# Optimization experiments

Hardware: AMD Instinct MI355X
Metric: run time of the kernel (lower is better)

Reference implementation:

```python
import jax, jax.numpy as jnp
import numpy as np

DEPTH, DIM, M_DIM, K = 3, 16, 16, 8  # depth, emb_dim, EGNN m_dim default, num_nearest_neighbors
LN_EPS = 1e-5


def _gather(x, idx):
    # x: [B,L,...], idx: [B,L,K] -> [B,L,K,...] (per-batch neighbor gather)
    return jax.vmap(lambda xb, ib: xb[ib])(x, idx)


def _lin(k, fi, fo):
    k1, k2 = jax.random.split(k)
    lim = 1.0 / np.sqrt(fi)
    w = jax.random.uniform(k1, (fi, fo), minval=-lim, maxval=lim, dtype=jnp.float32)
    b = jax.random.uniform(k2, (fo,), minval=-lim, maxval=lim, dtype=jnp.float32)
    return w, b


def _stacked(k, fi, fo):
    ws, bs = zip(*[_lin(kk, fi, fo) for kk in jax.random.split(k, DEPTH)])
    return jnp.stack(ws), jnp.stack(bs)


def setup_inputs() -> dict:
    key = jax.random.key(0)
    ks = jax.random.split(key, 16)
    B, L, num_tokens = 16, 1024, 2
    edge_in = 2 * DIM + 1  # feats_i, feats_j, rel_dist
    inp = {}
    inp['coords'] = jax.random.normal(ks[0], (B, L, 3), dtype=jnp.float32) * 3.0
    inp['residues'] = jax.random.randint(ks[1], (B, L), 0, num_tokens)
    inp['lengths'] = jax.random.randint(ks[2], (B,), L // 2, L + 1)
    inp['token_emb'] = jax.random.normal(ks[3], (num_tokens, DIM), dtype=jnp.float32)
    inp['pos_emb'] = jax.random.normal(ks[4], (L, DIM), dtype=jnp.float32)
    inp['edge_w1'], inp['edge_b1'] = _stacked(ks[5], edge_in, edge_in * 2)
    inp['edge_w2'], inp['edge_b2'] = _stacked(ks[6], edge_in * 2, M_DIM)
    inp['coors_w1'], inp['coors_b1'] = _stacked(ks[7], M_DIM, M_DIM * 4)
    inp['coors_w2'], inp['coors_b2'] = _stacked(ks[8], M_DIM * 4, 1)
    inp['ln_g'] = jnp.ones((DEPTH, DIM), jnp.float32)
    inp['ln_b'] = jnp.zeros((DEPTH, DIM), jnp.float32)
    inp['node_w1'], inp['node_b1'] = _stacked(ks[9], DIM + M_DIM, DIM * 2)
    inp['node_w2'], inp['node_b2'] = _stacked(ks[10], DIM * 2, DIM)
    inp['final_w'], inp['final_b'] = _lin(ks[11], DIM, 3)
    return inp


def reference(coords, residues, lengths, token_emb, pos_emb,
              edge_w1, edge_b1, edge_w2, edge_b2,
              coors_w1, coors_b1, coors_w2, coors_b2,
              ln_g, ln_b, node_w1, node_b1, node_w2, node_b2,
              final_w, final_b):
    B, L, _ = coords.shape
    silu = jax.nn.silu
    mask = jnp.arange(L)[None, :] < lengths[:, None]                 # [B,L]
    pair_mask = mask[:, :, None] & mask[:, None, :]                  # [B,L,L]
    eye = jnp.eye(L, dtype=bool)
    # chain adjacency: i <-> i+1 where both endpoints are within length
    r = jnp.arange(L - 1)
    chain = jnp.zeros((L, L), bool).at[r, r + 1].set(True)
    chain = chain | chain.T
    adj = (chain[None] & pair_mask) & ~eye                           # [B,L,L]

    feats = token_emb[residues] + pos_emb[None, :L]                  # [B,L,D]
    coors = coords
    for d in range(DEPTH):
        # pairwise squared distances for kNN ranking (memory-bound)
        rel_dist_full = jnp.sum((coors[:, :, None] - coors[:, None, :]) ** 2, -1)  # [B,L,L]
        ranking = jnp.where(pair_mask, rel_dist_full, 1e5)
        ranking = jnp.where(eye, -1.0, ranking)   # self always selected first
        ranking = jnp.where(adj, 0.0, ranking)    # adjacency edges forced in
        _, idx = jax.lax.top_k(-ranking, K)                           # [B,L,K] smallest
        mask_j = _gather(mask, idx)
        emask = mask[:, :, None] & mask_j                             # [B,L,K] (valid_radius=inf)
        coors_j = _gather(coors, idx)                                 # [B,L,K,3]
        rel_coors = coors[:, :, None] - coors_j                       # [B,L,K,3]
        rel_dist = jnp.sum(rel_coors ** 2, -1, keepdims=True)         # [B,L,K,1]
        feats_j = _gather(feats, idx)                                 # [B,L,K,D]
        feats_i = jnp.broadcast_to(feats[:, :, None], feats_j.shape)
        edge_in = jnp.concatenate([feats_i, feats_j, rel_dist], -1)   # [B,L,K,2D+1]
        h = silu(edge_in @ edge_w1[d] + edge_b1[d])
        m_ij = silu(h @ edge_w2[d] + edge_b2[d])                      # [B,L,K,M]
        # equivariant coordinate update
        w = silu(m_ij @ coors_w1[d] + coors_b1[d]) @ coors_w2[d] + coors_b2[d]
        w = jnp.where(emask[..., None], w, 0.0)[..., 0]               # [B,L,K]
        coors = coors + jnp.einsum('blk,blkc->blc', w, rel_coors)
        # node update (norm_feats=True in EGNN_Network -> LayerNorm)
        m_i = jnp.sum(jnp.where(emask[..., None], m_ij, 0.0), 2)      # [B,L,M]
        mu = feats.mean(-1, keepdims=True)
        var = jnp.mean((feats - mu) ** 2, -1, keepdims=True)
        normed = (feats - mu) / jnp.sqrt(var + LN_EPS) * ln_g[d] + ln_b[d]
        nin = jnp.concatenate([normed, m_i], -1)                      # [B,L,D+M]
        feats = feats + (silu(nin @ node_w1[d] + node_b1[d]) @ node_w2[d] + node_b2[d])
    delta = feats @ final_w + final_b                                 # [B,L,3]
    return delta
```

## Files before the change

### kernel.cpp

```cpp
#include <hip/hip_runtime.h>
#include <math.h>

typedef unsigned long long u64;
typedef unsigned int u32;

#define NB 16
#define SL 1024
#define DIM 16
#define MDIM 16
#define KNN 8
#define EH 66
#define CH 64
#define NHID 32
#define LN_EPS 1e-5f
#define W1T_STRIDE 36

__device__ __forceinline__ float silu_f(float x) {
    return x / (1.0f + __expf(-x));
}

__global__ __launch_bounds__(256) void init_kernel(
    const float* __restrict__ coords, const int* __restrict__ residues,
    const float* __restrict__ token_emb, const float* __restrict__ pos_emb,
    float* __restrict__ coordsA, float* __restrict__ featsA)
{
    const int nid = blockIdx.x * 256 + threadIdx.x;
    if (nid >= NB * SL) return;
    const int l = nid & (SL - 1);
    const int r = residues[nid];
#pragma unroll
    for (int c = 0; c < DIM; ++c)
        featsA[nid * DIM + c] = token_emb[r * DIM + c] + pos_emb[l * DIM + c];
#pragma unroll
    for (int c = 0; c < 3; ++c)
        coordsA[nid * 3 + c] = coords[nid * 3 + c];
}

__global__ __launch_bounds__(256) void pack_kernel(
    const float* __restrict__ ew1, const float* __restrict__ cw1,
    const float* __restrict__ nw1, const float* __restrict__ nw2,
    float* __restrict__ w1t, float* __restrict__ cw1t,
    float* __restrict__ nw1t, float* __restrict__ nw2t)
{
    const int stride = gridDim.x * 256;
    const int t0 = blockIdx.x * 256 + threadIdx.x;
    for (int idx = t0; idx < 3 * EH * 33; idx += stride) {
        int d = idx / (EH * 33); int r = idx - d * EH * 33; int u = r / 33; int c = r - u * 33;
        w1t[(d * EH + u) * W1T_STRIDE + c] = ew1[(d * 33 + c) * EH + u];
    }
    for (int idx = t0; idx < 3 * CH * 16; idx += stride) {
        int d = idx / (CH * 16); int r = idx - d * CH * 16; int t = r >> 4; int v = r & 15;
        cw1t[(d * CH + t) * 16 + v] = cw1[(d * 16 + v) * CH + t];
    }
    for (int idx = t0; idx < 3 * NHID * 32; idx += stride) {
        int d = idx / (NHID * 32); int r = idx - d * NHID * 32; int u = r >> 5; int c = r & 31;
        nw1t[(d * NHID + u) * 32 + c] = nw1[(d * 32 + c) * NHID + u];
    }
    for (int idx = t0; idx < 3 * 16 * 32; idx += stride) {
        int d = idx / (16 * 32); int r = idx - d * 16 * 32; int c = r >> 5; int u = r & 31;
        nw2t[(d * 16 + c) * 32 + u] = nw2[(d * 32 + u) * 16 + c];
    }
}

__device__ __forceinline__ void merge8(u32* a, const u32* bb) {
    u32 c[8];
#pragma unroll
    for (int t = 0; t < 8; ++t) c[t] = min(a[t], bb[7 - t]);
#define MCAS(x, y) { u32 mn = min(c[x], c[y]); u32 mx = max(c[x], c[y]); c[x] = mn; c[y] = mx; }
    MCAS(0, 4) MCAS(1, 5) MCAS(2, 6) MCAS(3, 7)
    MCAS(0, 2) MCAS(1, 3) MCAS(4, 6) MCAS(5, 7)
    MCAS(0, 1) MCAS(2, 3) MCAS(4, 5) MCAS(6, 7)
#undef MCAS
#pragma unroll
    for (int t = 0; t < 8; ++t) a[t] = c[t];
}

__global__ __launch_bounds__(1024) void knn_kernel(
    const float* __restrict__ coords, const int* __restrict__ lengths,
    int* __restrict__ idxbuf)
{
    __shared__ float s_cand[SL * 3];
    __shared__ u32 lists[16][64][9];
    const int tid = threadIdx.x;
    const int b = blockIdx.x >> 4;
    const int i0 = (blockIdx.x & 15) << 6;
    const int len = lengths[b];
    const float* cb = coords + (size_t)b * SL * 3;
    for (int idx = tid; idx < SL * 3; idx += 1024) s_cand[idx] = cb[idx];
    __syncthreads();

    const int wv = tid >> 6;
    const int lane = tid & 63;
    const int i = i0 + lane;
    const bool mi = i < len;
    const float xi = s_cand[i * 3 + 0], yi = s_cand[i * 3 + 1], zi = s_cand[i * 3 + 2];

    u32 lst[8];
#pragma unroll
    for (int t = 0; t < 8; ++t) lst[t] = 0xFFFFFFFFu;

    const int jbase = wv << 6;
#pragma unroll 4
    for (int jj = 0; jj < 64; ++jj) {
        const int j = jbase + jj;
        const float xj = s_cand[j * 3 + 0], yj = s_cand[j * 3 + 1], zj = s_cand[j * 3 + 2];
        const float dx = xi - xj, dy = yi - yj, dz = zi - zj;
        const float dist = dx * dx + dy * dy + dz * dz;
        const bool pm = mi && (j < len);
        float v = pm ? dist : 1e5f;
        v = (pm && (j - i == 1 || i - j == 1)) ? 0.0f : v;
        v = (j == i) ? -1.0f : v;
        u32 bits = __float_as_uint(v);
        bits ^= (u32)((int)bits >> 31) | 0x80000000u;
        const u32 key = (bits & 0xFFFFFC00u) | (u32)j;
#pragma unroll
        for (int p = 7; p >= 1; --p)
            lst[p] = (key < lst[p]) ? ((key < lst[p - 1]) ? lst[p - 1] : key) : lst[p];
        lst[0] = min(key, lst[0]);
    }

#pragma unroll
    for (int t = 0; t < 8; ++t) lists[wv][lane][t] = lst[t];
    __syncthreads();

    if (tid < 512) {
        const int p = tid >> 6, q = tid & 63;
        u32 a[8], bb[8];
#pragma unroll
        for (int t = 0; t < 8; ++t) { a[t] = lists[2 * p][q][t]; bb[t] = lists[2 * p + 1][q][t]; }
        merge8(a, bb);
#pragma unroll
        for (int t = 0; t < 8; ++t) lists[2 * p][q][t] = a[t];
    }
    __syncthreads();
    if (tid < 256) {
        const int p = tid >> 6, q = tid & 63;
        u32 a[8], bb[8];
#pragma unroll
        for (int t = 0; t < 8; ++t) { a[t] = lists[4 * p][q][t]; bb[t] = lists[4 * p + 2][q][t]; }
        merge8(a, bb);
#pragma unroll
        for (int t = 0; t < 8; ++t) lists[4 * p][q][t] = a[t];
    }
    __syncthreads();
    if (tid < 128) {
        const int p = tid >> 6, q = tid & 63;
        u32 a[8], bb[8];
#pragma unroll
        for (int t = 0; t < 8; ++t) { a[t] = lists[8 * p][q][t]; bb[t] = lists[8 * p + 4][q][t]; }
        merge8(a, bb);
#pragma unroll
        for (int t = 0; t < 8; ++t) lists[8 * p][q][t] = a[t];
    }
    __syncthreads();
    if (tid < 64) {
        const int q = tid;
        u32 a[8], bb[8];
#pragma unroll
        for (int t = 0; t < 8; ++t) { a[t] = lists[0][q][t]; bb[t] = lists[8][q][t]; }
        merge8(a, bb);
        const size_t node = (size_t)b * SL + i0 + q;
        int4 r0 = make_int4((int)(a[0] & 1023u), (int)(a[1] & 1023u), (int)(a[2] & 1023u), (int)(a[3] & 1023u));
        int4 r1 = make_int4((int)(a[4] & 1023u), (int)(a[5] & 1023u), (int)(a[6] & 1023u), (int)(a[7] & 1023u));
        ((int4*)idxbuf)[node * 2 + 0] = r0;
        ((int4*)idxbuf)[node * 2 + 1] = r1;
    }
}

__global__ __launch_bounds__(256, 4) void layer_kernel(
    const int d,
    const float* __restrict__ coordsIn, float* __restrict__ coordsOut,
    const float* __restrict__ featsIn, float* __restrict__ featsOut,
    const int* __restrict__ idxbuf, const int* __restrict__ lengths,
    const float* __restrict__ w1t, const float* __restrict__ g_eb1,
    const float* __restrict__ g_ew2, const float* __restrict__ g_eb2,
    const float* __restrict__ cw1t, const float* __restrict__ g_cb1,
    const float* __restrict__ g_cw2, const float* __restrict__ g_cb2,
    const float* __restrict__ g_lng, const float* __restrict__ g_lnb,
    const float* __restrict__ nw1t, const float* __restrict__ g_nb1,
    const float* __restrict__ nw2t, const float* __restrict__ g_nb2)
{
    __shared__ float s_w1[EH * 36];
    __shared__ float s_w2e[EH * 16];
    __shared__ float s_cw1[CH * 16];
    __shared__ float s_cw2v[CH];
    __shared__ float s_nw1[NHID * 36];
    __shared__ float s_nw2[16 * 36];
    __shared__ float s_eb1[EH], s_eb2[16], s_cb1[CH];
    __shared__ float s_lng[16], s_lnb[16], s_nb1[32], s_nb2[16];
    __shared__ float s_cb2v;
    __shared__ __align__(16) float s_ex[2 * 64 * 20];

    const int tid = threadIdx.x;
    for (int t = tid; t < EH * 36; t += 256) s_w1[t] = w1t[d * EH * 36 + t];
    for (int t = tid; t < EH * 16; t += 256) s_w2e[t] = g_ew2[d * EH * 16 + t];
    for (int t = tid; t < CH * 16; t += 256) s_cw1[t] = cw1t[d * CH * 16 + t];
    for (int t = tid; t < NHID * 32; t += 256) s_nw1[(t >> 5) * 36 + (t & 31)] = nw1t[d * NHID * 32 + t];
    for (int t = tid; t < 16 * 32; t += 256) s_nw2[(t >> 5) * 36 + (t & 31)] = nw2t[d * 16 * 32 + t];
    if (tid < CH) { s_cw2v[tid] = g_cw2[d * CH + tid]; s_cb1[tid] = g_cb1[d * CH + tid]; }
    if (tid < EH) s_eb1[tid] = g_eb1[d * EH + tid];
    if (tid < 16) {
        s_eb2[tid] = g_eb2[d * 16 + tid];
        s_lng[tid] = g_lng[d * 16 + tid];
        s_lnb[tid] = g_lnb[d * 16 + tid];
        s_nb2[tid] = g_nb2[d * 16 + tid];
    }
    if (tid < 32) s_nb1[tid] = g_nb1[d * 32 + tid];
    if (tid == 0) s_cb2v = g_cb2[d];

    const int wvid = tid >> 6;
    const int h = wvid & 1;
    const int p = wvid >> 1;
    const int lane = tid & 63;
    const int e = blockIdx.x * 128 + p * 64 + lane;
    const int n = e >> 3;
    const int b = n >> 10;
    const int i = n & (SL - 1);
    const int k = lane & 7;
    const int len = lengths[b];
    const int j = idxbuf[e];
    const bool em = (i < len) && (j < len);

    float fi[16], fj[16];
    {
        const float4* pp = (const float4*)(featsIn + (size_t)n * DIM);
        float4 a = pp[0], c2 = pp[1], c3 = pp[2], c4 = pp[3];
        fi[0]=a.x; fi[1]=a.y; fi[2]=a.z; fi[3]=a.w;
        fi[4]=c2.x; fi[5]=c2.y; fi[6]=c2.z; fi[7]=c2.w;
        fi[8]=c3.x; fi[9]=c3.y; fi[10]=c3.z; fi[11]=c3.w;
        fi[12]=c4.x; fi[13]=c4.y; fi[14]=c4.z; fi[15]=c4.w;
    }
    {
        const float4* pp = (const float4*)(featsIn + ((size_t)b * SL + j) * DIM);
        float4 a = pp[0], c2 = pp[1], c3 = pp[2], c4 = pp[3];
        fj[0]=a.x; fj[1]=a.y; fj[2]=a.z; fj[3]=a.w;
        fj[4]=c2.x; fj[5]=c2.y; fj[6]=c2.z; fj[7]=c2.w;
        fj[8]=c3.x; fj[9]=c3.y; fj[10]=c3.z; fj[11]=c3.w;
        fj[12]=c4.x; fj[13]=c4.y; fj[14]=c4.z; fj[15]=c4.w;
    }
    float ci[3], rel[3];
    {
        const float* cp = coordsIn + (size_t)n * 3;
        const float* cq = coordsIn + ((size_t)b * SL + j) * 3;
        ci[0] = cp[0]; ci[1] = cp[1]; ci[2] = cp[2];
        rel[0] = ci[0] - cq[0]; rel[1] = ci[1] - cq[1]; rel[2] = ci[2] - cq[2];
    }
    const float rd = fmaf(rel[0], rel[0], fmaf(rel[1], rel[1], rel[2] * rel[2]));

    __syncthreads();

    const int ub = h * 33;
    float macc[16];
#pragma unroll
    for (int v = 0; v < 16; ++v) macc[v] = h ? 0.0f : s_eb2[v];
#pragma unroll 3
    for (int uu = 0; uu < 33; ++uu) {
        const float* wr = &s_w1[(ub + uu) * 36];
        float h0 = s_eb1[ub + uu], h1 = 0.f, h2 = 0.f, h3 = 0.f;
#pragma unroll
        for (int c = 0; c < 16; c += 4) {
            h0 = fmaf(fi[c + 0], wr[c + 0], h0);
            h1 = fmaf(fi[c + 1], wr[c + 1], h1);
            h2 = fmaf(fi[c + 2], wr[c + 2], h2);
            h3 = fmaf(fi[c + 3], wr[c + 3], h3);
        }
#pragma unroll
        for (int c = 0; c < 16; c += 4) {
            h0 = fmaf(fj[c + 0], wr[16 + c + 0], h0);
            h1 = fmaf(fj[c + 1], wr[16 + c + 1], h1);
            h2 = fmaf(fj[c + 2], wr[16 + c + 2], h2);
            h3 = fmaf(fj[c + 3], wr[16 + c + 3], h3);
        }
        h0 = fmaf(rd, wr[32], h0);
        const float hh = silu_f((h0 + h1) + (h2 + h3));
        const float* w2r = &s_w2e[(ub + uu) * 16];
#pragma unroll
        for (int v = 0; v < 16; ++v) macc[v] = fmaf(hh, w2r[v], macc[v]);
    }

    float4* exq = (float4*)&s_ex[((p << 6) + lane) * 20];
    if (h) {
        exq[0] = make_float4(macc[0], macc[1], macc[2], macc[3]);
        exq[1] = make_float4(macc[4], macc[5], macc[6], macc[7]);
        exq[2] = make_float4(macc[8], macc[9], macc[10], macc[11]);
        exq[3] = make_float4(macc[12], macc[13], macc[14], macc[15]);
    }
    __syncthreads();
    float mm[16];
    if (!h) {
        float4 e0 = exq[0], e1 = exq[1], e2 = exq[2], e3 = exq[3];
        macc[0]+=e0.x; macc[1]+=e0.y; macc[2]+=e0.z; macc[3]+=e0.w;
        macc[4]+=e1.x; macc[5]+=e1.y; macc[6]+=e1.z; macc[7]+=e1.w;
        macc[8]+=e2.x; macc[9]+=e2.y; macc[10]+=e2.z; macc[11]+=e2.w;
        macc[12]+=e3.x; macc[13]+=e3.y; macc[14]+=e3.z; macc[15]+=e3.w;
#pragma unroll
        for (int v = 0; v < 16; ++v) mm[v] = silu_f(macc[v]);
        exq[0] = make_float4(mm[0], mm[1], mm[2], mm[3]);
        exq[1] = make_float4(mm[4], mm[5], mm[6], mm[7]);
        exq[2] = make_float4(mm[8], mm[9], mm[10], mm[11]);
        exq[3] = make_float4(mm[12], mm[13], mm[14], mm[15]);
    }
    __syncthreads();
    if (h) {
        float4 e0 = exq[0], e1 = exq[1], e2 = exq[2], e3 = exq[3];
        mm[0]=e0.x; mm[1]=e0.y; mm[2]=e0.z; mm[3]=e0.w;
        mm[4]=e1.x; mm[5]=e1.y; mm[6]=e1.z; mm[7]=e1.w;
        mm[8]=e2.x; mm[9]=e2.y; mm[10]=e2.z; mm[11]=e2.w;
        mm[12]=e3.x; mm[13]=e3.y; mm[14]=e3.z; mm[15]=e3.w;
    }

    const int tb = h * 32;
    float wa = 0.f;
#pragma unroll 4
    for (int tt = 0; tt < 32; ++tt) {
        const float* cr = &s_cw1[(tb + tt) * 16];
        float a0 = s_cb1[tb + tt], a1 = 0.f;
#pragma unroll
        for (int v = 0; v < 16; v += 2) {
            a0 = fmaf(mm[v], cr[v], a0);
            a1 = fmaf(mm[v + 1], cr[v + 1], a1);
        }
        wa = fmaf(silu_f(a0 + a1), s_cw2v[tb + tt], wa);
    }
    s_ex[((p << 6) + lane) * 20 + 16 + h] = wa;
    __syncthreads();
    const float wao = s_ex[((p << 6) + lane) * 20 + 17 - h];
    const float we = em ? (wa + wao + s_cb2v) : 0.f;

    float wr0 = we * rel[0], wr1 = we * rel[1], wr2 = we * rel[2];
#pragma unroll
    for (int s = 1; s < 8; s <<= 1) {
        wr0 += __shfl_xor(wr0, s, 64);
        wr1 += __shfl_xor(wr1, s, 64);
        wr2 += __shfl_xor(wr2, s, 64);
    }
    if (!h && k == 0) {
        coordsOut[(size_t)n * 3 + 0] = ci[0] + wr0;
        coordsOut[(size_t)n * 3 + 1] = ci[1] + wr1;
        coordsOut[(size_t)n * 3 + 2] = ci[2] + wr2;
    }

    float mi_[16];
#pragma unroll
    for (int v = 0; v < 16; ++v) mi_[v] = em ? mm[v] : 0.f;
#pragma unroll
    for (int s = 1; s < 8; s <<= 1) {
#pragma unroll
        for (int v = 0; v < 16; ++v) mi_[v] += __shfl_xor(mi_[v], s, 64);
    }

    float mu = 0.f;
#pragma unroll
    for (int c = 0; c < 16; ++c) mu += fi[c];
    mu *= 0.0625f;
    float var = 0.f;
#pragma unroll
    for (int c = 0; c < 16; ++c) { const float dd = fi[c] - mu; var = fmaf(dd, dd, var); }
    var *= 0.0625f;
    const float rs = rsqrtf(var + LN_EPS);
    float nn[16];
#pragma unroll
    for (int c = 0; c < 16; ++c) nn[c] = fmaf((fi[c] - mu) * rs, s_lng[c], s_lnb[c]);

    float nh[4];
#pragma unroll
    for (int q = 0; q < 4; ++q) {
        const int u = k * 4 + q;
        const float* nr = &s_nw1[u * 36];
        float a0 = s_nb1[u], a1 = 0.f;
#pragma unroll
        for (int c = 0; c < 16; c += 2) {
            a0 = fmaf(nn[c], nr[c], a0);
            a1 = fmaf(nn[c + 1], nr[c + 1], a1);
        }
#pragma unroll
        for (int v = 0; v < 16; v += 2) {
            a0 = fmaf(mi_[v], nr[16 + v], a0);
            a1 = fmaf(mi_[v + 1], nr[16 + v + 1], a1);
        }
        nh[q] = silu_f(a0 + a1);
    }

    const int c0 = 2 * k, c1 = 2 * k + 1;
    const float* w2a = &s_nw2[c0 * 36];
    const float* w2b = &s_nw2[c1 * 36];
    float o0 = s_nb2[c0], o1 = s_nb2[c1];
    const int lbase = lane & ~7;
#pragma unroll
    for (int u = 0; u < 32; ++u) {
        const float v = __shfl(nh[u & 3], lbase + (u >> 2), 64);
        o0 = fmaf(v, w2a[u], o0);
        o1 = fmaf(v, w2b[u], o1);
    }
    if (!h) {
        ((float2*)featsOut)[(size_t)n * 8 + k] = make_float2(fi[c0] + o0, fi[c1] + o1);
    }
}

__global__ __launch_bounds__(256) void final_kernel(
    const float* __restrict__ feats, const float* __restrict__ fw,
    const float* __restrict__ fb, float* __restrict__ out)
{
    const int nid = blockIdx.x * 256 + threadIdx.x;
    if (nid >= NB * SL) return;
    float f[DIM];
#pragma unroll
    for (int c = 0; c < DIM; ++c) f[c] = feats[nid * DIM + c];
#pragma unroll
    for (int o = 0; o < 3; ++o) {
        float acc = fb[o];
#pragma unroll
        for (int c = 0; c < DIM; ++c) acc = fmaf(f[c], fw[c * 3 + o], acc);
        out[nid * 3 + o] = acc;
    }
}

extern "C" void kernel_launch(void* const* d_in, const int* in_sizes, int n_in,
                              void* d_out, int out_size, void* d_ws, size_t ws_size,
                              hipStream_t stream) {
    const float* coords    = (const float*)d_in[0];
    const int*   residues  = (const int*)d_in[1];
    const int*   lengths   = (const int*)d_in[2];
    const float* token_emb = (const float*)d_in[3];
    const float* pos_emb   = (const float*)d_in[4];
    const float* ew1 = (const float*)d_in[5];
    const float* eb1 = (const float*)d_in[6];
    const float* ew2 = (const float*)d_in[7];
    const float* eb2 = (const float*)d_in[8];
    const float* cw1 = (const float*)d_in[9];
    const float* cb1 = (const float*)d_in[10];
    const float* cw2 = (const float*)d_in[11];
    const float* cb2 = (const float*)d_in[12];
    const float* lng = (const float*)d_in[13];
    const float* lnb = (const float*)d_in[14];
    const float* nw1 = (const float*)d_in[15];
    const float* nb1 = (const float*)d_in[16];
    const float* nw2 = (const float*)d_in[17];
    const float* nb2 = (const float*)d_in[18];
    const float* fw  = (const float*)d_in[19];
    const float* fb  = (const float*)d_in[20];

    float* ws = (float*)d_ws;
    float* coordsA = ws;
    float* coordsB = coordsA + NB * SL * 3;
    float* featsA  = coordsB + NB * SL * 3;
    float* featsB  = featsA + NB * SL * DIM;
    int*   idxbuf  = (int*)(featsB + NB * SL * DIM);
    float* w1t  = (float*)(idxbuf + NB * SL * KNN);
    float* cw1t = w1t + 3 * EH * W1T_STRIDE;
    float* nw1t = cw1t + 3 * CH * 16;
    float* nw2t = nw1t + 3 * NHID * 32;

    pack_kernel<<<32, 256, 0, stream>>>(ew1, cw1, nw1, nw2, w1t, cw1t, nw1t, nw2t);
    init_kernel<<<NB * SL / 256, 256, 0, stream>>>(coords, residues, token_emb, pos_emb, coordsA, featsA);

    float* cIn = coordsA; float* cOut = coordsB;
    float* fIn = featsA;  float* fOut = featsB;
    for (int d = 0; d < 3; ++d) {
        knn_kernel<<<NB * SL / 64, 1024, 0, stream>>>(cIn, lengths, idxbuf);
        layer_kernel<<<NB * SL * KNN / 128, 256, 0, stream>>>(d, cIn, cOut, fIn, fOut, idxbuf, lengths,
            w1t, eb1, ew2, eb2, cw1t, cb1, cw2, cb2, lng, lnb, nw1t, nb1, nw2t, nb2);
        float* t;
        t = cIn; cIn = cOut; cOut = t;
        t = fIn; fIn = fOut; fOut = t;
    }

    final_kernel<<<NB * SL / 256, 256, 0, stream>>>(fIn, fw, fb, (float*)d_out);
}
```

Measured before the change: 309.8 us.

## Precompute per-node edge-MLP first-layer projections to avoid per-edge matmul

```diff
diff --git a/kernel.cpp b/kernel.cpp
--- a/kernel.cpp
+++ b/kernel.cpp
@@ -9,11 +9,10 @@
 #define DIM 16
 #define MDIM 16
 #define KNN 8
-#define EH 66
 #define CH 64
 #define NHID 32
 #define LN_EPS 1e-5f
-#define W1T_STRIDE 36
+#define PST 144
 
 __device__ __forceinline__ float silu_f(float x) {
     return x / (1.0f + __expf(-x));
@@ -37,16 +36,28 @@
 }
 
 __global__ __launch_bounds__(256) void pack_kernel(
-    const float* __restrict__ ew1, const float* __restrict__ cw1,
+    const float* __restrict__ ew1, const float* __restrict__ ew2,
+    const float* __restrict__ cw1,
     const float* __restrict__ nw1, const float* __restrict__ nw2,
-    float* __restrict__ w1t, float* __restrict__ cw1t,
-    float* __restrict__ nw1t, float* __restrict__ nw2t)
+    float* __restrict__ w1tp, float* __restrict__ w1rp, float* __restrict__ w2p,
+    float* __restrict__ cw1t, float* __restrict__ nw1t, float* __restrict__ nw2t)
 {
     const int stride = gridDim.x * 256;
     const int t0 = blockIdx.x * 256 + threadIdx.x;
-    for (int idx = t0; idx < 3 * EH * 33; idx += stride) {
-        int d = idx / (EH * 33); int r = idx - d * EH * 33; int u = r / 33; int c = r - u * 33;
-        w1t[(d * EH + u) * W1T_STRIDE + c] = ew1[(d * 33 + c) * EH + u];
+    for (int idx = t0; idx < 3 * 132 * 16; idx += stride) {
+        int d = idx / (132 * 16); int r = idx - d * 132 * 16; int o = r >> 4; int c = r & 15;
+        int u = (o < 66) ? o : (o - 66);
+        int cc = (o < 66) ? c : (16 + c);
+        w1tp[idx] = ew1[(d * 33 + cc) * 66 + u];
+    }
+    for (int idx = t0; idx < 3 * 72; idx += stride) {
+        int d = idx / 72; int o = idx - d * 72; int hh = o / 36; int uu = o - hh * 36;
+        w1rp[idx] = (uu < 33) ? ew1[(d * 33 + 32) * 66 + hh * 33 + uu] : 0.0f;
+    }
+    for (int idx = t0; idx < 3 * 72 * 16; idx += stride) {
+        int d = idx / (72 * 16); int r = idx - d * 72 * 16; int u = r >> 4; int v = r & 15;
+        int hh = u / 36; int uu = u - hh * 36;
+        w2p[idx] = (uu < 33) ? ew2[(d * 66 + hh * 33 + uu) * 16 + v] : 0.0f;
     }
     for (int idx = t0; idx < 3 * CH * 16; idx += stride) {
         int d = idx / (CH * 16); int r = idx - d * CH * 16; int t = r >> 4; int v = r & 15;
@@ -60,6 +71,53 @@
         int d = idx / (16 * 32); int r = idx - d * 16 * 32; int c = r >> 5; int u = r & 31;
         nw2t[(d * 16 + c) * 32 + u] = nw2[(d * 32 + u) * 16 + c];
     }
+}
+
+__global__ __launch_bounds__(256) void phi_kernel(
+    const int d,
+    const float* __restrict__ feats,
+    const float* __restrict__ w1tp, const float* __restrict__ g_eb1,
+    float* __restrict__ P)
+{
+    __shared__ float s_wt[132 * 16];
+    __shared__ float s_b[66];
+    const int tid = threadIdx.x;
+    for (int t = tid; t < 132 * 16; t += 256) s_wt[t] = w1tp[d * 132 * 16 + t];
+    if (tid < 66) s_b[tid] = g_eb1[d * 66 + tid];
+    const int p = tid >> 6;
+    const int lane = tid & 63;
+    const int node = blockIdx.x * 64 + lane;
+    float f[16];
+    {
+        const float4* fp = (const float4*)(feats + (size_t)node * DIM);
+        float4 q0 = fp[0], q1 = fp[1], q2 = fp[2], q3 = fp[3];
+        f[0]=q0.x; f[1]=q0.y; f[2]=q0.z; f[3]=q0.w;
+        f[4]=q1.x; f[5]=q1.y; f[6]=q1.z; f[7]=q1.w;
+        f[8]=q2.x; f[9]=q2.y; f[10]=q2.z; f[11]=q2.w;
+        f[12]=q3.x; f[13]=q3.y; f[14]=q3.z; f[15]=q3.w;
+    }
+    __syncthreads();
+    const int obase = p * 33;
+    float res[36];
+    res[33] = 0.f; res[34] = 0.f; res[35] = 0.f;
+#pragma unroll 3
+    for (int oo = 0; oo < 33; ++oo) {
+        const float* wr = &s_wt[(obase + oo) * 16];
+        float a0 = (p < 2) ? s_b[obase + oo] : 0.0f;
+        float a1 = 0.f, a2 = 0.f, a3 = 0.f;
+#pragma unroll
+        for (int c = 0; c < 16; c += 4) {
+            a0 = fmaf(f[c + 0], wr[c + 0], a0);
+            a1 = fmaf(f[c + 1], wr[c + 1], a1);
+            a2 = fmaf(f[c + 2], wr[c + 2], a2);
+            a3 = fmaf(f[c + 3], wr[c + 3], a3);
+        }
+        res[oo] = (a0 + a1) + (a2 + a3);
+    }
+    float4* outp = (float4*)(P + (size_t)node * PST + p * 36);
+#pragma unroll
+    for (int q = 0; q < 9; ++q)
+        outp[q] = make_float4(res[4 * q + 0], res[4 * q + 1], res[4 * q + 2], res[4 * q + 3]);
 }
 
 __device__ __forceinline__ void merge8(u32* a, const u32* bb) {
@@ -171,34 +229,34 @@
     const int d,
     const float* __restrict__ coordsIn, float* __restrict__ coordsOut,
     const float* __restrict__ featsIn, float* __restrict__ featsOut,
+    const float* __restrict__ Pbuf,
     const int* __restrict__ idxbuf, const int* __restrict__ lengths,
-    const float* __restrict__ w1t, const float* __restrict__ g_eb1,
-    const float* __restrict__ g_ew2, const float* __restrict__ g_eb2,
+    const float* __restrict__ w1rp, const float* __restrict__ w2p,
+    const float* __restrict__ g_eb2,
     const float* __restrict__ cw1t, const float* __restrict__ g_cb1,
     const float* __restrict__ g_cw2, const float* __restrict__ g_cb2,
     const float* __restrict__ g_lng, const float* __restrict__ g_lnb,
     const float* __restrict__ nw1t, const float* __restrict__ g_nb1,
     const float* __restrict__ nw2t, const float* __restrict__ g_nb2)
 {
-    __shared__ float s_w1[EH * 36];
-    __shared__ float s_w2e[EH * 16];
+    __shared__ float s_w2e[72 * 16];
+    __shared__ float s_w1r[72];
     __shared__ float s_cw1[CH * 16];
     __shared__ float s_cw2v[CH];
     __shared__ float s_nw1[NHID * 36];
     __shared__ float s_nw2[16 * 36];
-    __shared__ float s_eb1[EH], s_eb2[16], s_cb1[CH];
+    __shared__ float s_eb2[16], s_cb1[CH];
     __shared__ float s_lng[16], s_lnb[16], s_nb1[32], s_nb2[16];
     __shared__ float s_cb2v;
     __shared__ __align__(16) float s_ex[2 * 64 * 20];
 
     const int tid = threadIdx.x;
-    for (int t = tid; t < EH * 36; t += 256) s_w1[t] = w1t[d * EH * 36 + t];
-    for (int t = tid; t < EH * 16; t += 256) s_w2e[t] = g_ew2[d * EH * 16 + t];
+    for (int t = tid; t < 72 * 16; t += 256) s_w2e[t] = w2p[d * 72 * 16 + t];
     for (int t = tid; t < CH * 16; t += 256) s_cw1[t] = cw1t[d * CH * 16 + t];
     for (int t = tid; t < NHID * 32; t += 256) s_nw1[(t >> 5) * 36 + (t & 31)] = nw1t[d * NHID * 32 + t];
     for (int t = tid; t < 16 * 32; t += 256) s_nw2[(t >> 5) * 36 + (t & 31)] = nw2t[d * 16 * 32 + t];
+    if (tid < 72) s_w1r[tid] = w1rp[d * 72 + tid];
     if (tid < CH) { s_cw2v[tid] = g_cw2[d * CH + tid]; s_cb1[tid] = g_cb1[d * CH + tid]; }
-    if (tid < EH) s_eb1[tid] = g_eb1[d * EH + tid];
     if (tid < 16) {
         s_eb2[tid] = g_eb2[d * 16 + tid];
         s_lng[tid] = g_lng[d * 16 + tid];
@@ -221,7 +279,7 @@
     const int j = idxbuf[e];
     const bool em = (i < len) && (j < len);
 
-    float fi[16], fj[16];
+    float fi[16];
     {
         const float4* pp = (const float4*)(featsIn + (size_t)n * DIM);
         float4 a = pp[0], c2 = pp[1], c3 = pp[2], c4 = pp[3];
@@ -230,14 +288,6 @@
         fi[8]=c3.x; fi[9]=c3.y; fi[10]=c3.z; fi[11]=c3.w;
         fi[12]=c4.x; fi[13]=c4.y; fi[14]=c4.z; fi[15]=c4.w;
     }
-    {
-        const float4* pp = (const float4*)(featsIn + ((size_t)b * SL + j) * DIM);
-        float4 a = pp[0], c2 = pp[1], c3 = pp[2], c4 = pp[3];
-        fj[0]=a.x; fj[1]=a.y; fj[2]=a.z; fj[3]=a.w;
-        fj[4]=c2.x; fj[5]=c2.y; fj[6]=c2.z; fj[7]=c2.w;
-        fj[8]=c3.x; fj[9]=c3.y; fj[10]=c3.z; fj[11]=c3.w;
-        fj[12]=c4.x; fj[13]=c4.y; fj[14]=c4.z; fj[15]=c4.w;
-    }
     float ci[3], rel[3];
     {
         const float* cp = coordsIn + (size_t)n * 3;
@@ -247,35 +297,38 @@
     }
     const float rd = fmaf(rel[0], rel[0], fmaf(rel[1], rel[1], rel[2] * rel[2]));
 
-    __syncthreads();
-
-    const int ub = h * 33;
+    const int ub = h * 36;
+    const float* PiP = Pbuf + (size_t)n * PST + ub;
+    const float* PjP = Pbuf + ((size_t)b * SL + j) * PST + 72 + ub;
+    float4 pa = *(const float4*)PiP;
+    float4 pb = *(const float4*)PjP;
+
+    __syncthreads();
+
     float macc[16];
 #pragma unroll
     for (int v = 0; v < 16; ++v) macc[v] = h ? 0.0f : s_eb2[v];
-#pragma unroll 3
-    for (int uu = 0; uu < 33; ++uu) {
-        const float* wr = &s_w1[(ub + uu) * 36];
-        float h0 = s_eb1[ub + uu], h1 = 0.f, h2 = 0.f, h3 = 0.f;
-#pragma unroll
-        for (int c = 0; c < 16; c += 4) {
-            h0 = fmaf(fi[c + 0], wr[c + 0], h0);
-            h1 = fmaf(fi[c + 1], wr[c + 1], h1);
-            h2 = fmaf(fi[c + 2], wr[c + 2], h2);
-            h3 = fmaf(fi[c + 3], wr[c + 3], h3);
+#pragma unroll
+    for (int c4 = 0; c4 < 9; ++c4) {
+        float4 na, nb;
+        if (c4 < 8) {
+            na = *(const float4*)(PiP + 4 * (c4 + 1));
+            nb = *(const float4*)(PjP + 4 * (c4 + 1));
         }
-#pragma unroll
-        for (int c = 0; c < 16; c += 4) {
-            h0 = fmaf(fj[c + 0], wr[16 + c + 0], h0);
-            h1 = fmaf(fj[c + 1], wr[16 + c + 1], h1);
-            h2 = fmaf(fj[c + 2], wr[16 + c + 2], h2);
-            h3 = fmaf(fj[c + 3], wr[16 + c + 3], h3);
+        const int u0 = ub + c4 * 4;
+        const float hu0 = silu_f(fmaf(rd, s_w1r[u0 + 0], pa.x + pb.x));
+        const float hu1 = silu_f(fmaf(rd, s_w1r[u0 + 1], pa.y + pb.y));
+        const float hu2 = silu_f(fmaf(rd, s_w1r[u0 + 2], pa.z + pb.z));
+        const float hu3 = silu_f(fmaf(rd, s_w1r[u0 + 3], pa.w + pb.w));
+        const float* w2r = &s_w2e[u0 * 16];
+#pragma unroll
+        for (int v = 0; v < 16; ++v) {
+            float m0 = fmaf(hu0, w2r[v], macc[v]);
+            float m1 = fmaf(hu1, w2r[16 + v], m0);
+            float m2 = fmaf(hu2, w2r[32 + v], m1);
+            macc[v] = fmaf(hu3, w2r[48 + v], m2);
         }
-        h0 = fmaf(rd, wr[32], h0);
-        const float hh = silu_f((h0 + h1) + (h2 + h3));
-        const float* w2r = &s_w2e[(ub + uu) * 16];
-#pragma unroll
-        for (int v = 0; v < 16; ++v) macc[v] = fmaf(hh, w2r[v], macc[v]);
+        if (c4 < 8) { pa = na; pb = nb; }
     }
 
     float4* exq = (float4*)&s_ex[((p << 6) + lane) * 20];
@@ -446,20 +499,24 @@
     float* featsA  = coordsB + NB * SL * 3;
     float* featsB  = featsA + NB * SL * DIM;
     int*   idxbuf  = (int*)(featsB + NB * SL * DIM);
-    float* w1t  = (float*)(idxbuf + NB * SL * KNN);
-    float* cw1t = w1t + 3 * EH * W1T_STRIDE;
+    float* w1tp = (float*)(idxbuf + NB * SL * KNN);
+    float* w1rp = w1tp + 3 * 132 * 16;
+    float* w2p  = w1rp + 3 * 72;
+    float* cw1t = w2p + 3 * 72 * 16;
     float* nw1t = cw1t + 3 * CH * 16;
     float* nw2t = nw1t + 3 * NHID * 32;
-
-    pack_kernel<<<32, 256, 0, stream>>>(ew1, cw1, nw1, nw2, w1t, cw1t, nw1t, nw2t);
+    float* Pbuf = nw2t + 3 * 16 * 32;
+
+    pack_kernel<<<32, 256, 0, stream>>>(ew1, ew2, cw1, nw1, nw2, w1tp, w1rp, w2p, cw1t, nw1t, nw2t);
     init_kernel<<<NB * SL / 256, 256, 0, stream>>>(coords, residues, token_emb, pos_emb, coordsA, featsA);
 
     float* cIn = coordsA; float* cOut = coordsB;
     float* fIn = featsA;  float* fOut = featsB;
     for (int d = 0; d < 3; ++d) {
         knn_kernel<<<NB * SL / 64, 1024, 0, stream>>>(cIn, lengths, idxbuf);
-        layer_kernel<<<NB * SL * KNN / 128, 256, 0, stream>>>(d, cIn, cOut, fIn, fOut, idxbuf, lengths,
-            w1t, eb1, ew2, eb2, cw1t, cb1, cw2, cb2, lng, lnb, nw1t, nb1, nw2t, nb2);
+        phi_kernel<<<NB * SL / 64, 256, 0, stream>>>(d, fIn, w1tp, eb1, Pbuf);
+        layer_kernel<<<NB * SL * KNN / 128, 256, 0, stream>>>(d, cIn, cOut, fIn, fOut, Pbuf, idxbuf, lengths,
+            w1rp, w2p, eb2, cw1t, cb1, cw2, cb2, lng, lnb, nw1t, nb1, nw2t, nb2);
         float* t;
         t = cIn; cIn = cOut; cOut = t;
         t = fIn; fIn = fOut; fOut = t;
```

After: 321.2 us. 1.04x slower.
